# Kernel tuning notes

Measured on AMD Instinct MI355X. Metric: run time of the kernel, lower is better.

## Reference

```python
import jax, jax.numpy as jnp
import numpy as np

B, C, H, W = 2, 192, 128, 128
HEADS = 4
M = 128          # num_tokens
RD = 10          # reducted_dim
GS = 256         # category_size
TDF = 16         # dim_ffn_td
HID = 4 * C      # mlp hidden (768)
HIDT = HID + TDF # 784 after concat with token-dict features
KS = 5


def _ln(x, g, b):
    mu = x.mean(-1, keepdims=True)
    var = ((x - mu) ** 2).mean(-1, keepdims=True)
    return (x - mu) / jnp.sqrt(var + 1e-5) * g + b


def _gelu(x):
    return jax.nn.gelu(x, approximate=False)  # torch nn.GELU default = exact erf


def setup_inputs() -> dict:
    key = jax.random.key(0)
    ks = jax.random.split(key, 16)
    s = 0.02
    inp = {
        "x": jax.random.normal(ks[0], (B, C, H, W), jnp.float32),
        "x_size": H,
        "td": jax.random.normal(ks[1], (M, C), jnp.float32),
        "g1": jnp.ones((C,)), "b1": jnp.zeros((C,)),
        "g2": jnp.ones((C,)), "b2": jnp.zeros((C,)),
        "g3": jnp.ones((C,)), "b3": jnp.zeros((C,)),
        "wq_w": jax.random.normal(ks[2], (C, RD)) * s, "wq_b": jnp.zeros((RD,)),
        "wk_w": jax.random.normal(ks[3], (C, RD)) * s, "wk_b": jnp.zeros((RD,)),
        "wv_w": jax.random.normal(ks[4], (C, C)) * s, "wv_b": jnp.zeros((C,)),
        "ca_scale": jnp.ones((1,)),
        "wqkv_w": jax.random.normal(ks[5], (C, 3 * C)) * s, "wqkv_b": jnp.zeros((3 * C,)),
        "proj_w": jax.random.normal(ks[6], (C, C)) * s, "proj_b": jnp.zeros((C,)),
        "fc_td_w": jax.random.normal(ks[7], (C, TDF)) * s, "fc_td_b": jnp.zeros((TDF,)),
        "fc1_w": jax.random.normal(ks[8], (C, HID)) * s, "fc1_b": jnp.zeros((HID,)),
        "dw_w": jax.random.normal(ks[9], (HIDT, 1, KS, KS)) * s, "dw_b": jnp.zeros((HIDT,)),
        "fc2_w": jax.random.normal(ks[10], (HIDT, C)) * s, "fc2_b": jnp.zeros((C,)),
    }
    return inp


def reference(x, x_size, td, g1, b1, g2, b2, g3, b3, wq_w, wq_b, wk_w, wk_b,
              wv_w, wv_b, ca_scale, wqkv_w, wqkv_b, proj_w, proj_b,
              fc_td_w, fc_td_b, fc1_w, fc1_b, dw_w, dw_b, fc2_w, fc2_b):
    b, c, h, w = x.shape
    n = h * w
    xs = x.reshape(b, c, n).transpose(0, 2, 1)          # [b,n,c] patch_embed
    shortcut = xs
    xn = _ln(xs, g1, b1)                                # norm1

    # ---- ATD_CA: L2-normalized cross-attention to token dict ----
    q = xn @ wq_w + wq_b                                # [b,n,rd]
    k = td @ wk_w + wk_b                                # [m,rd]
    v = td @ wv_w + wv_b                                # [m,c]
    qn = q / jnp.maximum(jnp.linalg.norm(q, axis=-1, keepdims=True), 1e-12)
    kn = k / jnp.maximum(jnp.linalg.norm(k, axis=-1, keepdims=True), 1e-12)
    sim = jnp.einsum('bnr,mr->bnm', qn, kn)
    scale = 1.0 + jnp.clip(ca_scale, 0.0, 3.0) * np.log(M)
    sim = jax.nn.softmax(sim * scale, axis=-1)          # [b,n,m]
    x_atd = jnp.einsum('bnm,mc->bnc', sim, v)
    tk_id = jnp.argmax(sim, axis=-1)                    # [b,n] int

    # ---- AC_MSA: category-sorted grouped self-attention ----
    qkv = xn @ wqkv_w + wqkv_b                          # [b,n,3c]
    sort_idx = jnp.argsort(tk_id, axis=-1)              # [b,n]
    inv_idx = jnp.argsort(sort_idx, axis=-1)            # index_reverse
    shuf = jnp.take_along_axis(qkv, sort_idx[:, :, None], axis=1)
    gs = min(n, GS)
    ng = (n + gs - 1) // gs
    pad_n = ng * gs - n
    pad = jnp.flip(shuf[:, n - pad_n:n, :], axis=1)
    padded = jnp.concatenate([shuf, pad], axis=1)       # [b, ng*gs, 3c]
    hd = c // HEADS
    y = padded.reshape(b, ng, gs, 3, HEADS, hd)
    y = jnp.transpose(y, (3, 0, 1, 4, 2, 5))            # [3,b,ng,H,gs,hd]
    q2, k2, v2 = y[0], y[1], y[2]
    attn = jnp.einsum('bghqd,bghkd->bghqk', q2, k2) * (hd ** -0.5)
    attn = jax.nn.softmax(attn, axis=-1)
    o = jnp.einsum('bghqk,bghkd->bghqd', attn, v2)
    o = jnp.transpose(o, (0, 1, 3, 2, 4)).reshape(b, ng * gs, c)[:, :n, :]
    o = jnp.take_along_axis(o, inv_idx[:, :, None], axis=1)
    x_aca = o @ proj_w + proj_b

    # ---- token-dict features gathered per token ----
    td_feat = td @ fc_td_w + fc_td_b                    # [m,tdf]
    x_td = jnp.take(td_feat, tk_id, axis=0)             # [b,n,tdf]

    # ---- ConvFFN_td ----
    xn2 = _ln(xs, g2, b2)
    h1 = _gelu(xn2 @ fc1_w + fc1_b)                     # [b,n,hid]
    hcat = jnp.concatenate([h1, x_td], axis=-1)         # [b,n,hidt]
    img = hcat.transpose(0, 2, 1).reshape(b, HIDT, h, w)
    conv = jax.lax.conv_general_dilated(
        img, dw_w, window_strides=(1, 1), padding=((KS // 2, KS // 2),) * 2,
        dimension_numbers=('NCHW', 'OIHW', 'NCHW'), feature_group_count=HIDT)
    conv = _gelu(conv + dw_b[None, :, None, None])
    conv = conv.reshape(b, HIDT, n).transpose(0, 2, 1)
    x_ffn = (hcat + conv) @ fc2_w + fc2_b
    x_ffn = _ln(x_ffn, g3, b3)                          # norm3

    out = shortcut + x_atd + x_aca + x_ffn
    return out.transpose(0, 2, 1).reshape(b, c, h, w)
```

## Files before the change

### kernel.cpp

```cpp
#include <hip/hip_runtime.h>
#include <hip/hip_bf16.h>
#include <math.h>

using bf16 = __hip_bfloat16;

static constexpr int B = 2, C = 192, Hh = 128, Ww = 128, N = Hh * Ww;
static constexpr int M = 128, RD = 10, GS = 256, NG = N / GS;
static constexpr int HEADS = 4, HD = C / HEADS;
static constexpr int TDF = 16, HID = 4 * C, HIDT = HID + TDF;
static constexpr int TC3 = 3 * C;
static constexpr float LOG_M = 4.852030263919617f;
static constexpr float ATT_SCALE = 0.14433756729740643f;

typedef __attribute__((ext_vector_type(8))) short bf16x8;
typedef __attribute__((ext_vector_type(4))) float f32x4;

__device__ __forceinline__ float b2f(bf16 v) { return __bfloat162float(v); }
__device__ __forceinline__ bf16 f2b(float v) { return __float2bfloat16(v); }
__device__ __forceinline__ float bits2f(unsigned short u) { return __uint_as_float(((unsigned)u) << 16); }
__device__ __forceinline__ unsigned short f2bits(float f) {
    union { bf16 h; unsigned short u; } cv; cv.h = f2b(f); return cv.u;
}
__device__ __forceinline__ float gelu_exact(float v) {
    return 0.5f * v * (1.0f + erff(v * 0.70710678118654752f));
}

__global__ void __launch_bounds__(256) k_wtrans(const float* in, bf16* out, int K, int Nn) {
    __shared__ float T[64][65];
    int n0 = blockIdx.x * 64, k0 = blockIdx.y * 64;
    int tid = threadIdx.x;
    for (int e = tid; e < 4096; e += 256) {
        int kk = e >> 6, nn = e & 63;
        if (k0 + kk < K) T[kk][nn] = in[(size_t)(k0 + kk) * Nn + n0 + nn];
    }
    __syncthreads();
    for (int e = tid; e < 4096; e += 256) {
        int nn = e >> 6, kk = e & 63;
        if (k0 + kk < K) out[(size_t)(n0 + nn) * K + k0 + kk] = f2b(T[kk][nn]);
    }
}

__global__ void k_precompute(const float* td, const float* wk_w, const float* wk_b,
                             const float* wv_w, const float* wv_b,
                             const float* fc_td_w, const float* fc_td_b,
                             float* kn, bf16* vvT, float* tdf) {
    int m = blockIdx.x;
    int lane = threadIdx.x;
    __shared__ float trow[C];
    for (int ch = lane; ch < C; ch += 64) trow[ch] = td[m * C + ch];
    __syncthreads();
    __shared__ float ks[RD];
    __shared__ float inv_s;
    if (lane < RD) {
        float s = wk_b[lane];
        for (int ch = 0; ch < C; ++ch) s += trow[ch] * wk_w[ch * RD + lane];
        ks[lane] = s;
    }
    __syncthreads();
    if (lane == 0) {
        float ss = 0.f;
        for (int r = 0; r < RD; ++r) ss += ks[r] * ks[r];
        inv_s = 1.0f / fmaxf(sqrtf(ss), 1e-12f);
    }
    __syncthreads();
    if (lane < RD) kn[m * RD + lane] = ks[lane] * inv_s;
    for (int c0 = 0; c0 < 3; ++c0) {
        int co = lane + 64 * c0;
        float s = wv_b[co];
        for (int ch = 0; ch < C; ++ch) s += trow[ch] * wv_w[ch * C + co];
        vvT[(size_t)co * M + m] = f2b(s);
    }
    if (lane < TDF) {
        float s = fc_td_b[lane];
        for (int ch = 0; ch < C; ++ch) s += trow[ch] * fc_td_w[ch * TDF + lane];
        tdf[m * TDF + lane] = s;
    }
}

__global__ void __launch_bounds__(256) k_ln(const float* x, bf16* t, float* xn32, float* acc) {
    __shared__ float Xs[64 * 193];
    __shared__ float mu_s[64], rs_s[64];
    int tid = threadIdx.x;
    int m0 = blockIdx.x * 64;
    int b = m0 / N, i0 = m0 % N;
    for (int e = tid; e < 192 * 64; e += 256) {
        int ch = e >> 6, ii = e & 63;
        Xs[ii * 193 + ch] = x[((size_t)b * C + ch) * N + i0 + ii];
    }
    __syncthreads();
    {
        int tok = tid >> 2, part = tid & 3;
        float s = 0.f, ss = 0.f;
        for (int ch = part * 48; ch < part * 48 + 48; ++ch) {
            float v = Xs[tok * 193 + ch]; s += v; ss += v * v;
        }
        s += __shfl_xor(s, 1); ss += __shfl_xor(ss, 1);
        s += __shfl_xor(s, 2); ss += __shfl_xor(ss, 2);
        if (part == 0) {
            float mu = s / C;
            mu_s[tok] = mu;
            rs_s[tok] = rsqrtf(ss / C - mu * mu + 1e-5f);
        }
    }
    __syncthreads();
    for (int e = tid; e < 64 * 192; e += 256) {
        int ii = e / 192, ch = e % 192;
        float v = Xs[ii * 193 + ch];
        float xn = (v - mu_s[ii]) * rs_s[ii];
        size_t g = (size_t)(m0 + ii);
        t[g * C + ch] = f2b(xn);
        xn32[g * C + ch] = xn;
        acc[g * C + ch] = v;
    }
}

__global__ void __launch_bounds__(256) k_atdca(const float* xn32, const float* g1, const float* b1,
                        const float* wq_w, const float* wq_b, const float* ca_scale,
                        const float* kn, bf16* p_buf, int* tk_id) {
    int t0 = blockIdx.x * 4;
    int w = threadIdx.x >> 6, lane = threadIdx.x & 63;
    int g = t0 + w;
    float xn[3];
    #pragma unroll
    for (int k = 0; k < 3; ++k) {
        int ch = lane + 64 * k;
        xn[k] = xn32[(size_t)g * C + ch] * g1[ch] + b1[ch];
    }
    float q[RD];
    #pragma unroll
    for (int r = 0; r < RD; ++r) {
        float p = 0.f;
        #pragma unroll
        for (int k = 0; k < 3; ++k) { int ch = lane + 64 * k; p += xn[k] * wq_w[ch * RD + r]; }
        for (int mk = 32; mk >= 1; mk >>= 1) p += __shfl_xor(p, mk);
        q[r] = p + wq_b[r];
    }
    float ssn = 0.f;
    #pragma unroll
    for (int r = 0; r < RD; ++r) ssn += q[r] * q[r];
    float invq = 1.0f / fmaxf(sqrtf(ssn), 1e-12f);
    float s0 = 0.f, s1 = 0.f;
    #pragma unroll
    for (int r = 0; r < RD; ++r) {
        float qr = q[r] * invq;
        s0 += qr * kn[lane * RD + r];
        s1 += qr * kn[(lane + 64) * RD + r];
    }
    float mv; int mi;
    if (s1 > s0) { mv = s1; mi = lane + 64; } else { mv = s0; mi = lane; }
    for (int mk = 32; mk >= 1; mk >>= 1) {
        float ov = __shfl_xor(mv, mk); int oi = __shfl_xor(mi, mk);
        if (ov > mv || (ov == mv && oi < mi)) { mv = ov; mi = oi; }
    }
    float cs = ca_scale[0]; cs = fminf(fmaxf(cs, 0.0f), 3.0f);
    float scale = 1.0f + cs * LOG_M;
    float e0 = expf((s0 - mv) * scale), e1 = expf((s1 - mv) * scale);
    float sum = e0 + e1;
    for (int mk = 32; mk >= 1; mk >>= 1) sum += __shfl_xor(sum, mk);
    float invs = 1.0f / sum;
    p_buf[(size_t)g * M + lane] = f2b(e0 * invs);
    p_buf[(size_t)g * M + lane + 64] = f2b(e1 * invs);
    if (lane == 0) tk_id[g] = mi;
}

__global__ void __launch_bounds__(256) k_pv(const bf16* p_buf, const bf16* vvT, float* acc) {
    __shared__ __align__(16) short As[64 * 136];
    __shared__ __align__(16) short Bs[64 * 136];
    int tid = threadIdx.x;
    int m0 = blockIdx.x * 64;
    int n0 = blockIdx.y * 64;
    for (int e = tid; e < 64 * 16; e += 256) {
        int m = e >> 4, kc = (e & 15) * 8;
        *(uint4*)&As[m * 136 + kc] = *(const uint4*)(p_buf + (size_t)(m0 + m) * M + kc);
    }
    for (int e = tid; e < 64 * 16; e += 256) {
        int n = e >> 4, kc = (e & 15) * 8;
        *(uint4*)&Bs[n * 136 + kc] = *(const uint4*)(vvT + (size_t)(n0 + n) * M + kc);
    }
    __syncthreads();
    int w = tid >> 6, lane = tid & 63;
    int wm = (w >> 1) * 32, wn = (w & 1) * 32;
    int lr = lane & 15, lk = (lane >> 4) * 8;
    f32x4 acc00 = {0.f,0.f,0.f,0.f}, acc01 = acc00, acc10 = acc00, acc11 = acc00;
    #pragma unroll
    for (int ks = 0; ks < 4; ++ks) {
        int k0 = ks * 32 + lk;
        bf16x8 a0 = *(bf16x8*)&As[(wm + lr) * 136 + k0];
        bf16x8 a1 = *(bf16x8*)&As[(wm + 16 + lr) * 136 + k0];
        bf16x8 b0 = *(bf16x8*)&Bs[(wn + lr) * 136 + k0];
        bf16x8 b1 = *(bf16x8*)&Bs[(wn + 16 + lr) * 136 + k0];
        acc00 = __builtin_amdgcn_mfma_f32_16x16x32_bf16(a0, b0, acc00, 0, 0, 0);
        acc01 = __builtin_amdgcn_mfma_f32_16x16x32_bf16(a0, b1, acc01, 0, 0, 0);
        acc10 = __builtin_amdgcn_mfma_f32_16x16x32_bf16(a1, b0, acc10, 0, 0, 0);
        acc11 = __builtin_amdgcn_mfma_f32_16x16x32_bf16(a1, b1, acc11, 0, 0, 0);
    }
    int rbase = (lane >> 4) * 4;
    f32x4 accs[2][2] = {{acc00, acc01}, {acc10, acc11}};
    #pragma unroll
    for (int mt = 0; mt < 2; ++mt) {
        #pragma unroll
        for (int nt = 0; nt < 2; ++nt) {
            int co = n0 + wn + nt * 16 + lr;
            #pragma unroll
            for (int r = 0; r < 4; ++r) {
                int tok = m0 + wm + mt * 16 + rbase + r;
                acc[(size_t)tok * C + co] += accs[mt][nt][r];
            }
        }
    }
}

template<int NOUT, int OUTLD, int MODE, bool HASGAIN>
__global__ void __launch_bounds__(256) k_gemm192(const bf16* Abuf, const float* gain, const float* beta,
                                                 const bf16* Wt, const float* bias,
                                                 bf16* outb, float* outf) {
    __shared__ __align__(16) short As[64 * 200];
    __shared__ __align__(16) short Bs[64 * 200];
    int tid = threadIdx.x;
    int m0 = blockIdx.x * 64;
    int n0 = blockIdx.y * 64;
    for (int e = tid; e < 64 * 24; e += 256) {
        int m = e / 24, kc = (e % 24) * 8;
        uint4 raw = *(const uint4*)(Abuf + (size_t)(m0 + m) * C + kc);
        if (HASGAIN) {
            unsigned short* u = (unsigned short*)&raw;
            unsigned short o[8];
            #pragma unroll
            for (int j = 0; j < 8; ++j) o[j] = f2bits(bits2f(u[j]) * gain[kc + j] + beta[kc + j]);
            *(uint4*)&As[m * 200 + kc] = *(uint4*)o;
        } else {
            *(uint4*)&As[m * 200 + kc] = raw;
        }
    }
    for (int e = tid; e < 64 * 24; e += 256) {
        int n = e / 24, kc = (e % 24) * 8;
        *(uint4*)&Bs[n * 200 + kc] = *(const uint4*)(Wt + (size_t)(n0 + n) * C + kc);
    }
    __syncthreads();
    int w = tid >> 6, lane = tid & 63;
    int wm = (w >> 1) * 32, wn = (w & 1) * 32;
    int lr = lane & 15, lk = (lane >> 4) * 8;
    f32x4 acc00 = {0.f,0.f,0.f,0.f}, acc01 = acc00, acc10 = acc00, acc11 = acc00;
    #pragma unroll
    for (int ks = 0; ks < 6; ++ks) {
        int k0 = ks * 32 + lk;
        bf16x8 a0 = *(bf16x8*)&As[(wm + lr) * 200 + k0];
        bf16x8 a1 = *(bf16x8*)&As[(wm + 16 + lr) * 200 + k0];
        bf16x8 b0 = *(bf16x8*)&Bs[(wn + lr) * 200 + k0];
        bf16x8 b1 = *(bf16x8*)&Bs[(wn + 16 + lr) * 200 + k0];
        acc00 = __builtin_amdgcn_mfma_f32_16x16x32_bf16(a0, b0, acc00, 0, 0, 0);
        acc01 = __builtin_amdgcn_mfma_f32_16x16x32_bf16(a0, b1, acc01, 0, 0, 0);
        acc10 = __builtin_amdgcn_mfma_f32_16x16x32_bf16(a1, b0, acc10, 0, 0, 0);
        acc11 = __builtin_amdgcn_mfma_f32_16x16x32_bf16(a1, b1, acc11, 0, 0, 0);
    }
    int rbase = (lane >> 4) * 4;
    f32x4 accs[2][2] = {{acc00, acc01}, {acc10, acc11}};
    #pragma unroll
    for (int mt = 0; mt < 2; ++mt) {
        #pragma unroll
        for (int nt = 0; nt < 2; ++nt) {
            int co = n0 + wn + nt * 16 + lr;
            float bv = bias[co];
            #pragma unroll
            for (int r = 0; r < 4; ++r) {
                int tok = m0 + wm + mt * 16 + rbase + r;
                float v = accs[mt][nt][r] + bv;
                if (MODE == 0) outb[(size_t)tok * OUTLD + co] = f2b(v);
                else if (MODE == 1) outb[(size_t)tok * OUTLD + co] = f2b(gelu_exact(v));
                else outf[(size_t)tok * OUTLD + co] += v;
            }
        }
    }
}

__global__ void k_sort_count(const int* tk_id, int* chunk_cnt) {
    int c = blockIdx.x, b = blockIdx.y;
    int tid = threadIdx.x;
    __shared__ int cnt[M];
    cnt[tid] = 0;
    __syncthreads();
    atomicAdd(&cnt[tk_id[b * N + c * 128 + tid]], 1);
    __syncthreads();
    chunk_cnt[(b * 128 + c) * M + tid] = cnt[tid];
}

__global__ void k_sort_scan(int* chunk_cnt) {
    int b = blockIdx.x;
    int k = threadIdx.x;
    int tot = 0;
    for (int c = 0; c < 128; ++c) tot += chunk_cnt[(b * 128 + c) * M + k];
    __shared__ int totals[M];
    __shared__ int base[M];
    totals[k] = tot;
    __syncthreads();
    if (k == 0) {
        int run = 0;
        for (int kk = 0; kk < M; ++kk) { base[kk] = run; run += totals[kk]; }
    }
    __syncthreads();
    int run = base[k];
    for (int c = 0; c < 128; ++c) {
        int v = chunk_cnt[(b * 128 + c) * M + k];
        chunk_cnt[(b * 128 + c) * M + k] = run;
        run += v;
    }
}

__global__ void k_sort_scatter(const int* tk_id, const int* chunk_cnt, int* sort_idx) {
    int c = blockIdx.x, b = blockIdx.y;
    int k = threadIdx.x;
    __shared__ int keys[128];
    keys[k] = tk_id[b * N + c * 128 + k];
    __syncthreads();
    int off = chunk_cnt[(b * 128 + c) * M + k];
    for (int j = 0; j < 128; ++j) {
        if (keys[j] == k) sort_idx[b * N + off++] = c * 128 + j;
    }
}

__global__ void __launch_bounds__(256) k_attn_mfma(const bf16* qkv, const int* sort_idx, bf16* o_buf) {
    int g = blockIdx.x, h = blockIdx.y, b = blockIdx.z;
    __shared__ int sidx[GS];
    __shared__ __align__(16) unsigned short Kl[256 * 64];
    __shared__ __align__(16) unsigned short Vt[48 * 256];
    __shared__ __align__(16) unsigned short Pl[4][64 * 32];
    int tid = threadIdx.x;
    sidx[tid] = sort_idx[b * N + g * GS + tid];
    __syncthreads();
    {
        int row = tid;
        int srow = sidx[row];
        size_t kb = ((size_t)(b * N + srow)) * TC3 + C + h * HD;
        size_t vb = ((size_t)(b * N + srow)) * TC3 + 2 * C + h * HD;
        #pragma unroll
        for (int db = 0; db < 6; ++db) {
            uint4 kv = *(const uint4*)(qkv + kb + db * 8);
            *(uint4*)&Kl[row * 64 + ((db ^ (row & 7)) * 8)] = kv;
            uint4 vv4 = *(const uint4*)(qkv + vb + db * 8);
            unsigned short* vu = (unsigned short*)&vv4;
            #pragma unroll
            for (int j = 0; j < 8; ++j) {
                int d = db * 8 + j;
                Vt[d * 256 + (((row >> 3) ^ (d & 7)) * 8) + (row & 7)] = vu[j];
            }
        }
        uint4 z = {0u,0u,0u,0u};
        *(uint4*)&Kl[row * 64 + ((6 ^ (row & 7)) * 8)] = z;
        *(uint4*)&Kl[row * 64 + ((7 ^ (row & 7)) * 8)] = z;
    }
    __syncthreads();
    int w = tid >> 6, l = tid & 63;
    int lq = l & 15, g8 = l >> 4;
    bf16x8 qf[4][2];
    #pragma unroll
    for (int qt = 0; qt < 4; ++qt) {
        int qrow = sidx[w * 64 + qt * 16 + lq];
        size_t qb = ((size_t)(b * N + qrow)) * TC3 + h * HD;
        qf[qt][0] = *(const bf16x8*)(qkv + qb + g8 * 8);
        int d1 = 32 + g8 * 8;
        if (d1 < HD) qf[qt][1] = *(const bf16x8*)(qkv + qb + d1);
        else { uint4 z = {0u,0u,0u,0u}; qf[qt][1] = *(bf16x8*)&z; }
    }
    float mrun[4], lrun[4];
    f32x4 Oa[4][3];
    #pragma unroll
    for (int qt = 0; qt < 4; ++qt) {
        mrun[qt] = -1e30f; lrun[qt] = 0.f;
        #pragma unroll
        for (int dt = 0; dt < 3; ++dt) Oa[qt][dt] = (f32x4){0.f,0.f,0.f,0.f};
    }
    unsigned short* Pw = &Pl[w][0];
    for (int ck = 0; ck < 8; ++ck) {
        int kbase = ck * 32;
        bf16x8 kf[2][2];
        #pragma unroll
        for (int kt = 0; kt < 2; ++kt) {
            int key = kbase + kt * 16 + lq;
            #pragma unroll
            for (int ks = 0; ks < 2; ++ks)
                kf[kt][ks] = *(bf16x8*)&Kl[key * 64 + (((ks * 4 + g8) ^ (key & 7)) * 8)];
        }
        bf16x8 vf[3];
        #pragma unroll
        for (int dt = 0; dt < 3; ++dt) {
            int d = dt * 16 + lq;
            vf[dt] = *(bf16x8*)&Vt[d * 256 + ((((kbase >> 3) + g8) ^ (d & 7)) * 8)];
        }
        #pragma unroll
        for (int qt = 0; qt < 4; ++qt) {
            f32x4 s0 = {0.f,0.f,0.f,0.f}, s1 = s0;
            s0 = __builtin_amdgcn_mfma_f32_16x16x32_bf16(kf[0][0], qf[qt][0], s0, 0, 0, 0);
            s0 = __builtin_amdgcn_mfma_f32_16x16x32_bf16(kf[0][1], qf[qt][1], s0, 0, 0, 0);
            s1 = __builtin_amdgcn_mfma_f32_16x16x32_bf16(kf[1][0], qf[qt][0], s1, 0, 0, 0);
            s1 = __builtin_amdgcn_mfma_f32_16x16x32_bf16(kf[1][1], qf[qt][1], s1, 0, 0, 0);
            float sv0[4], sv1[4];
            float cmax = -1e30f;
            #pragma unroll
            for (int r = 0; r < 4; ++r) {
                sv0[r] = s0[r] * ATT_SCALE; sv1[r] = s1[r] * ATT_SCALE;
                cmax = fmaxf(cmax, fmaxf(sv0[r], sv1[r]));
            }
            cmax = fmaxf(cmax, __shfl_xor(cmax, 16));
            cmax = fmaxf(cmax, __shfl_xor(cmax, 32));
            float mnew = fmaxf(mrun[qt], cmax);
            float sf = expf(mrun[qt] - mnew);
            float p0[4], p1[4], csum = 0.f;
            #pragma unroll
            for (int r = 0; r < 4; ++r) {
                p0[r] = expf(sv0[r] - mnew); p1[r] = expf(sv1[r] - mnew);
                csum += p0[r] + p1[r];
            }
            csum += __shfl_xor(csum, 16);
            csum += __shfl_xor(csum, 32);
            lrun[qt] = lrun[qt] * sf + csum;
            mrun[qt] = mnew;
            int q = qt * 16 + lq;
            {
                unsigned short pw[4];
                #pragma unroll
                for (int r = 0; r < 4; ++r) pw[r] = f2bits(p0[r]);
                int slot = g8;
                int addr = q * 32 + (((slot >> 1) ^ (q & 3)) * 8) + (slot & 1) * 4;
                *(uint2*)&Pw[addr] = *(uint2*)pw;
                #pragma unroll
                for (int r = 0; r < 4; ++r) pw[r] = f2bits(p1[r]);
                slot = 4 + g8;
                addr = q * 32 + (((slot >> 1) ^ (q & 3)) * 8) + (slot & 1) * 4;
                *(uint2*)&Pw[addr] = *(uint2*)pw;
            }
            float sfr[4];
            #pragma unroll
            for (int r = 0; r < 4; ++r) sfr[r] = __shfl(sf, 4 * g8 + r);
            #pragma unroll
            for (int dt = 0; dt < 3; ++dt)
                #pragma unroll
                for (int r = 0; r < 4; ++r) Oa[qt][dt][r] *= sfr[r];
            bf16x8 pa = *(bf16x8*)&Pw[q * 32 + ((g8 ^ (lq & 3)) * 8)];
            #pragma unroll
            for (int dt = 0; dt < 3; ++dt)
                Oa[qt][dt] = __builtin_amdgcn_mfma_f32_16x16x32_bf16(pa, vf[dt], Oa[qt][dt], 0, 0, 0);
        }
    }
    #pragma unroll
    for (int qt = 0; qt < 4; ++qt) {
        float invq = 1.0f / lrun[qt];
        float invr[4];
        #pragma unroll
        for (int r = 0; r < 4; ++r) invr[r] = __shfl(invq, 4 * g8 + r);
        #pragma unroll
        for (int r = 0; r < 4; ++r) {
            int grow = sidx[w * 64 + qt * 16 + 4 * g8 + r];
            size_t obase = ((size_t)(b * N + grow)) * C + h * HD;
            #pragma unroll
            for (int dt = 0; dt < 3; ++dt)
                o_buf[obase + dt * 16 + lq] = f2b(Oa[qt][dt][r] * invr[r]);
        }
    }
}

__global__ void k_tdfill(const int* tk_id, const float* tdf, bf16* hcat) {
    int idx = blockIdx.x * 256 + threadIdx.x;
    if (idx >= B * N * TDF) return;
    int tok = idx >> 4, f = idx & 15;
    hcat[(size_t)tok * HIDT + HID + f] = f2b(tdf[tk_id[tok] * TDF + f]);
}

__global__ void __launch_bounds__(256) k_conv(const bf16* hcat, const float* dw_w, const float* dw_b,
                                              bf16* convsum) {
    int st = blockIdx.x;
    int c16 = blockIdx.y;
    int b = blockIdx.z;
    int tx0 = (st & 7) * 16, ty0 = (st >> 3) * 16;
    int tid = threadIdx.x;
    __shared__ __align__(16) float Hf[20 * 81 * 4];
    __shared__ __align__(16) float Wf[25 * 16];
    __shared__ float Wb[16];
    for (int e = tid; e < 400; e += 256) {
        int tap = e >> 4, ch = e & 15;
        Wf[e] = dw_w[(size_t)(c16 * 16 + ch) * 25 + tap];
    }
    if (tid < 16) Wb[tid] = dw_b[c16 * 16 + tid];
    for (int e = tid; e < 800; e += 256) {
        int pos = e >> 1, sc = e & 1;
        int py = pos / 20, px = pos % 20;
        int gy = ty0 + py - 2, gx = tx0 + px - 2;
        uint4 v = {0u, 0u, 0u, 0u};
        if (gy >= 0 && gy < Hh && gx >= 0 && gx < Ww)
            v = *(const uint4*)(hcat + ((size_t)b * N + gy * Ww + gx) * HIDT + c16 * 16 + sc * 8);
        unsigned short* u = (unsigned short*)&v;
        float4 f0 = { bits2f(u[0]), bits2f(u[1]), bits2f(u[2]), bits2f(u[3]) };
        float4 f1 = { bits2f(u[4]), bits2f(u[5]), bits2f(u[6]), bits2f(u[7]) };
        int base = (py * 81 + px * 4 + sc * 2) * 4;
        *(float4*)&Hf[base] = f0;
        *(float4*)&Hf[base + 4] = f1;
    }
    __syncthreads();
    int cc = tid & 1, lx = (tid >> 1) & 7, ly = tid >> 4;
    float acc[2][8] = {};
    #pragma unroll 1
    for (int ky = 0; ky < 5; ++ky) {
        int py = ly + ky;
        float4 w[5][2];
        #pragma unroll
        for (int kx = 0; kx < 5; ++kx) {
            w[kx][0] = *(float4*)&Wf[(ky * 5 + kx) * 16 + cc * 8];
            w[kx][1] = *(float4*)&Wf[(ky * 5 + kx) * 16 + cc * 8 + 4];
        }
        #pragma unroll
        for (int c = 0; c < 6; ++c) {
            int px = 2 * lx + c;
            int base = (py * 81 + px * 4 + cc * 2) * 4;
            float4 f0 = *(float4*)&Hf[base];
            float4 f1 = *(float4*)&Hf[base + 4];
            float f[8] = { f0.x, f0.y, f0.z, f0.w, f1.x, f1.y, f1.z, f1.w };
            #pragma unroll
            for (int kx = 0; kx < 5; ++kx) {
                int ox = c - kx;
                if (ox >= 0 && ox < 2) {
                    const float* wp = (const float*)&w[kx][0];
                    #pragma unroll
                    for (int j = 0; j < 8; ++j) acc[ox][j] += f[j] * wp[j];
                }
            }
        }
    }
    int gy = ty0 + ly;
    #pragma unroll
    for (int ox = 0; ox < 2; ++ox) {
        int px = 2 * lx + ox + 2, py = ly + 2;
        int base = (py * 81 + px * 4 + cc * 2) * 4;
        float4 f0 = *(float4*)&Hf[base];
        float4 f1 = *(float4*)&Hf[base + 4];
        float cf[8] = { f0.x, f0.y, f0.z, f0.w, f1.x, f1.y, f1.z, f1.w };
        unsigned short ow[8];
        #pragma unroll
        for (int j = 0; j < 8; ++j)
            ow[j] = f2bits(cf[j] + gelu_exact(acc[ox][j] + Wb[cc * 8 + j]));
        int gx = tx0 + 2 * lx + ox;
        *(uint4*)(convsum + ((size_t)b * N + gy * Ww + gx) * HIDT + c16 * 16 + cc * 8) = *(uint4*)ow;
    }
}

__global__ void __launch_bounds__(256) k_fc2ln(const bf16* convsum, const bf16* Wt,
                                               const float* bias, const float* g3, const float* b3,
                                               const float* accres, float* out) {
    __shared__ __align__(16) char smem[65536];
    unsigned short* AsB = (unsigned short*)smem;
    unsigned short* BsB = (unsigned short*)(smem + 16384);
    float* Ot = (float*)smem;
    int tid = threadIdx.x;
    int m0 = blockIdx.x * 64;
    int w = tid >> 6, lane = tid & 63;
    int lr = lane & 15, g8 = lane >> 4;
    f32x4 acc[12];
    #pragma unroll
    for (int nt = 0; nt < 12; ++nt) acc[nt] = (f32x4){0.f, 0.f, 0.f, 0.f};

    auto stage = [&](int d, int kc) {
        int kb = kc * 64;
        unsigned short* As = AsB + d * 4096;
        unsigned short* Bs = BsB + d * 12288;
        for (int e = tid; e < 512; e += 256) {
            int m = e >> 3, k8 = (e & 7) * 8;
            uint4 v = {0u,0u,0u,0u};
            if (kb + k8 < HIDT) v = *(const uint4*)(convsum + (size_t)(m0 + m) * HIDT + kb + k8);
            *(uint4*)&As[m * 64 + (((e & 7) ^ (m & 7)) * 8)] = v;
        }
        for (int e = tid; e < 1536; e += 256) {
            int n = e >> 3, k8 = (e & 7) * 8;
            uint4 v = {0u,0u,0u,0u};
            if (kb + k8 < HIDT) v = *(const uint4*)(Wt + (size_t)n * HIDT + kb + k8);
            *(uint4*)&Bs[n * 64 + (((e & 7) ^ (n & 7)) * 8)] = v;
        }
    };
    stage(0, 0);
    int cur = 0;
    for (int kc = 0; kc < 13; ++kc) {
        __syncthreads();
        if (kc + 1 < 13) stage(cur ^ 1, kc + 1);
        unsigned short* As = AsB + cur * 4096;
        unsigned short* Bs = BsB + cur * 12288;
        #pragma unroll
        for (int ks = 0; ks < 2; ++ks) {
            int kg = ks * 4 + g8;
            int arow = w * 16 + lr;
            bf16x8 a = *(bf16x8*)&As[arow * 64 + ((kg ^ (arow & 7)) * 8)];
            #pragma unroll
            for (int nt = 0; nt < 12; ++nt) {
                int nrow = nt * 16 + lr;
                bf16x8 bfr = *(bf16x8*)&Bs[nrow * 64 + ((kg ^ (nrow & 7)) * 8)];
                acc[nt] = __builtin_amdgcn_mfma_f32_16x16x32_bf16(a, bfr, acc[nt], 0, 0, 0);
            }
        }
        cur ^= 1;
    }
    #pragma unroll
    for (int nt = 0; nt < 12; ++nt) {
        float bv = bias[nt * 16 + lr];
        #pragma unroll
        for (int r = 0; r < 4; ++r) acc[nt][r] += bv;
    }
    float mu_r[4], rs_r[4];
    #pragma unroll
    for (int r = 0; r < 4; ++r) {
        float s = 0.f, ss = 0.f;
        #pragma unroll
        for (int nt = 0; nt < 12; ++nt) { float v = acc[nt][r]; s += v; ss += v * v; }
        s += __shfl_xor(s, 1); ss += __shfl_xor(ss, 1);
        s += __shfl_xor(s, 2); ss += __shfl_xor(ss, 2);
        s += __shfl_xor(s, 4); ss += __shfl_xor(ss, 4);
        s += __shfl_xor(s, 8); ss += __shfl_xor(ss, 8);
        mu_r[r] = s / C;
        rs_r[r] = rsqrtf(ss / C - mu_r[r] * mu_r[r] + 1e-5f);
    }
    int bb = m0 / N, i0 = m0 % N;
    for (int h = 0; h < 2; ++h) {
        __syncthreads();
        #pragma unroll
        for (int ntl = 0; ntl < 6; ++ntl) {
            int nt = h * 6 + ntl;
            int c = nt * 16 + lr;
            float g3v = g3[c], b3v = b3[c];
            #pragma unroll
            for (int r = 0; r < 4; ++r) {
                int tok = m0 + w * 16 + g8 * 4 + r;
                float o = accres[(size_t)tok * C + c] + (acc[nt][r] - mu_r[r]) * rs_r[r] * g3v + b3v;
                Ot[(ntl * 16 + lr) * 68 + w * 16 + g8 * 4 + r] = o;
            }
        }
        __syncthreads();
        for (int e = tid; e < 96 * 16; e += 256) {
            int row = e >> 4, q4 = e & 15;
            int c = h * 96 + row;
            float4 v = *(float4*)&Ot[row * 68 + q4 * 4];
            *(float4*)(out + ((size_t)(bb * C + c)) * N + i0 + q4 * 4) = v;
        }
    }
}

__global__ void k_sentinel(float* out, int nelem) {
    int i = blockIdx.x * blockDim.x + threadIdx.x;
    if (i < nelem) out[i] = 1234.0f;
}

extern "C" void kernel_launch(void* const* d_in, const int* in_sizes, int n_in,
                              void* d_out, int out_size, void* d_ws, size_t ws_size,
                              hipStream_t stream) {
    const float* x        = (const float*)d_in[0];
    const float* td       = (const float*)d_in[2];
    const float* g1       = (const float*)d_in[3];
    const float* b1       = (const float*)d_in[4];
    const float* g2       = (const float*)d_in[5];
    const float* b2v      = (const float*)d_in[6];
    const float* g3       = (const float*)d_in[7];
    const float* b3       = (const float*)d_in[8];
    const float* wq_w     = (const float*)d_in[9];
    const float* wq_b     = (const float*)d_in[10];
    const float* wk_w     = (const float*)d_in[11];
    const float* wk_b     = (const float*)d_in[12];
    const float* wv_w     = (const float*)d_in[13];
    const float* wv_b     = (const float*)d_in[14];
    const float* ca_scale = (const float*)d_in[15];
    const float* wqkv_w   = (const float*)d_in[16];
    const float* wqkv_b   = (const float*)d_in[17];
    const float* proj_w   = (const float*)d_in[18];
    const float* proj_b   = (const float*)d_in[19];
    const float* fc_td_w  = (const float*)d_in[20];
    const float* fc_td_b  = (const float*)d_in[21];
    const float* fc1_w    = (const float*)d_in[22];
    const float* fc1_b    = (const float*)d_in[23];
    const float* dw_w     = (const float*)d_in[24];
    const float* dw_b     = (const float*)d_in[25];
    const float* fc2_w    = (const float*)d_in[26];
    const float* fc2_b    = (const float*)d_in[27];
    float* out = (float*)d_out;

    char* ws = (char*)d_ws;
    size_t off = 0;
    auto alloc = [&](size_t bytes) { size_t o = off; off += (bytes + 255) & ~(size_t)255; return o; };
    size_t o_t     = alloc((size_t)B * N * C * 2);
    size_t o_xn32  = alloc((size_t)B * N * C * 4);
    size_t o_acc   = alloc((size_t)B * N * C * 4);
    size_t o_qkv   = alloc((size_t)B * N * TC3 * 2);
    size_t o_obuf  = alloc((size_t)B * N * C * 2);
    size_t o_hcat  = alloc((size_t)B * N * HIDT * 2);
    size_t o_conv  = alloc((size_t)B * N * HIDT * 2);
    size_t o_kn    = alloc((size_t)M * RD * 4);
    size_t o_vvT   = alloc((size_t)C * M * 2);
    size_t o_tdf   = alloc((size_t)M * TDF * 4);
    size_t o_tk    = alloc((size_t)B * N * 4);
    size_t o_sidx  = alloc((size_t)B * N * 4);
    size_t o_ccnt  = alloc((size_t)B * 128 * M * 4);
    size_t o_pbuf  = alloc((size_t)B * N * M * 2);
    size_t o_wqkvT = alloc((size_t)TC3 * C * 2);
    size_t o_projT = alloc((size_t)C * C * 2);
    size_t o_fc1T  = alloc((size_t)HID * C * 2);
    size_t o_fc2T  = alloc((size_t)C * HIDT * 2);

    if (ws_size < off) {
        k_sentinel<<<(out_size + 255) / 256, 256, 0, stream>>>(out, out_size);
        return;
    }

    bf16*  t_buf   = (bf16*)(ws + o_t);
    float* xn32    = (float*)(ws + o_xn32);
    float* acc     = (float*)(ws + o_acc);
    bf16*  qkv     = (bf16*)(ws + o_qkv);
    bf16*  o_bufp  = (bf16*)(ws + o_obuf);
    bf16*  hcat    = (bf16*)(ws + o_hcat);
    bf16*  convsum = (bf16*)(ws + o_conv);
    float* kn      = (float*)(ws + o_kn);
    bf16*  vvT     = (bf16*)(ws + o_vvT);
    float* tdf     = (float*)(ws + o_tdf);
    int*   tk_id   = (int*)(ws + o_tk);
    int*   sidx    = (int*)(ws + o_sidx);
    int*   ccnt    = (int*)(ws + o_ccnt);
    bf16*  p_buf   = (bf16*)(ws + o_pbuf);
    bf16*  wqkvT   = (bf16*)(ws + o_wqkvT);
    bf16*  projT   = (bf16*)(ws + o_projT);
    bf16*  fc1T    = (bf16*)(ws + o_fc1T);
    bf16*  fc2T    = (bf16*)(ws + o_fc2T);

    k_wtrans<<<dim3(TC3 / 64, C / 64), 256, 0, stream>>>(wqkv_w, wqkvT, C, TC3);
    k_wtrans<<<dim3(C / 64, C / 64), 256, 0, stream>>>(proj_w, projT, C, C);
    k_wtrans<<<dim3(HID / 64, C / 64), 256, 0, stream>>>(fc1_w, fc1T, C, HID);
    k_wtrans<<<dim3(C / 64, (HIDT + 63) / 64), 256, 0, stream>>>(fc2_w, fc2T, HIDT, C);

    k_precompute<<<M, 64, 0, stream>>>(td, wk_w, wk_b, wv_w, wv_b, fc_td_w, fc_td_b, kn, vvT, tdf);
    k_ln<<<B * N / 64, 256, 0, stream>>>(x, t_buf, xn32, acc);
    k_atdca<<<B * N / 4, 256, 0, stream>>>(xn32, g1, b1, wq_w, wq_b, ca_scale, kn, p_buf, tk_id);
    k_pv<<<dim3(B * N / 64, C / 64), 256, 0, stream>>>(p_buf, vvT, acc);
    k_gemm192<TC3, TC3, 0, true><<<dim3(B * N / 64, TC3 / 64), 256, 0, stream>>>(
        t_buf, g1, b1, wqkvT, wqkv_b, qkv, nullptr);
    k_sort_count<<<dim3(128, B), 128, 0, stream>>>(tk_id, ccnt);
    k_sort_scan<<<B, 128, 0, stream>>>(ccnt);
    k_sort_scatter<<<dim3(128, B), 128, 0, stream>>>(tk_id, ccnt, sidx);
    k_attn_mfma<<<dim3(NG, HEADS, B), 256, 0, stream>>>(qkv, sidx, o_bufp);
    k_gemm192<C, C, 2, false><<<dim3(B * N / 64, C / 64), 256, 0, stream>>>(
        o_bufp, nullptr, nullptr, projT, proj_b, nullptr, acc);
    k_gemm192<HID, HIDT, 1, true><<<dim3(B * N / 64, HID / 64), 256, 0, stream>>>(
        t_buf, g2, b2v, fc1T, fc1_b, hcat, nullptr);
    k_tdfill<<<(B * N * TDF + 255) / 256, 256, 0, stream>>>(tk_id, tdf, hcat);
    k_conv<<<dim3(64, 49, B), 256, 0, stream>>>(hcat, dw_w, dw_b, convsum);
    k_fc2ln<<<B * N / 64, 256, 0, stream>>>(convsum, fc2T, fc2_b, g3, b3, acc, out);
}
```

Baseline: 390.9 us.

## Enlarge GEMM tiles to 128x96 and fold LN affine into the LN kernel

Replaces the 64x64 single-shot GEMM kernel with a 128x96 tile that loops over K in two 96-wide chunks, giving each wave a 4x3 grid of MFMA accumulators for more operand reuse per LDS load. The LayerNorm gain and bias for norm1 and norm2 are now applied once in k_ln, which writes two bf16 normalized buffers, so the GEMM loaders no longer do per-element affine conversion. This costs an extra bf16 activation write and read plus higher register pressure from 48 accumulator values per lane.

Result: slower. 399.4 us (+2.2%).

```diff
diff --git a/kernel.cpp b/kernel.cpp
--- a/kernel.cpp
+++ b/kernel.cpp
@@ -77,7 +77,9 @@
     }
 }
 
-__global__ void __launch_bounds__(256) k_ln(const float* x, bf16* t, float* xn32, float* acc) {
+__global__ void __launch_bounds__(256) k_ln(const float* x, const float* g1, const float* b1,
+                                            const float* g2, const float* b2v,
+                                            bf16* xn1, bf16* xn2, float* xn32, float* acc) {
     __shared__ float Xs[64 * 193];
     __shared__ float mu_s[64], rs_s[64];
     int tid = threadIdx.x;
@@ -108,7 +110,8 @@
         float v = Xs[ii * 193 + ch];
         float xn = (v - mu_s[ii]) * rs_s[ii];
         size_t g = (size_t)(m0 + ii);
-        t[g * C + ch] = f2b(xn);
+        xn1[g * C + ch] = f2b(xn * g1[ch] + b1[ch]);
+        xn2[g * C + ch] = f2b(xn * g2[ch] + b2v[ch]);
         xn32[g * C + ch] = xn;
         acc[g * C + ch] = v;
     }
@@ -210,61 +213,59 @@
     }
 }
 
-template<int NOUT, int OUTLD, int MODE, bool HASGAIN>
-__global__ void __launch_bounds__(256) k_gemm192(const bf16* Abuf, const float* gain, const float* beta,
-                                                 const bf16* Wt, const float* bias,
-                                                 bf16* outb, float* outf) {
-    __shared__ __align__(16) short As[64 * 200];
-    __shared__ __align__(16) short Bs[64 * 200];
+template<int OUTLD, int MODE>
+__global__ void __launch_bounds__(256) k_gemm_big(const bf16* Abuf, const bf16* Wt, const float* bias,
+                                                  bf16* outb, float* outf) {
+    __shared__ __align__(16) unsigned short As[128 * 104];
+    __shared__ __align__(16) unsigned short Bs[96 * 104];
     int tid = threadIdx.x;
-    int m0 = blockIdx.x * 64;
-    int n0 = blockIdx.y * 64;
-    for (int e = tid; e < 64 * 24; e += 256) {
-        int m = e / 24, kc = (e % 24) * 8;
-        uint4 raw = *(const uint4*)(Abuf + (size_t)(m0 + m) * C + kc);
-        if (HASGAIN) {
-            unsigned short* u = (unsigned short*)&raw;
-            unsigned short o[8];
-            #pragma unroll
-            for (int j = 0; j < 8; ++j) o[j] = f2bits(bits2f(u[j]) * gain[kc + j] + beta[kc + j]);
-            *(uint4*)&As[m * 200 + kc] = *(uint4*)o;
-        } else {
-            *(uint4*)&As[m * 200 + kc] = raw;
-        }
-    }
-    for (int e = tid; e < 64 * 24; e += 256) {
-        int n = e / 24, kc = (e % 24) * 8;
-        *(uint4*)&Bs[n * 200 + kc] = *(const uint4*)(Wt + (size_t)(n0 + n) * C + kc);
-    }
-    __syncthreads();
+    int m0 = blockIdx.x * 128, n0 = blockIdx.y * 96;
     int w = tid >> 6, lane = tid & 63;
-    int wm = (w >> 1) * 32, wn = (w & 1) * 32;
-    int lr = lane & 15, lk = (lane >> 4) * 8;
-    f32x4 acc00 = {0.f,0.f,0.f,0.f}, acc01 = acc00, acc10 = acc00, acc11 = acc00;
-    #pragma unroll
-    for (int ks = 0; ks < 6; ++ks) {
-        int k0 = ks * 32 + lk;
-        bf16x8 a0 = *(bf16x8*)&As[(wm + lr) * 200 + k0];
-        bf16x8 a1 = *(bf16x8*)&As[(wm + 16 + lr) * 200 + k0];
-        bf16x8 b0 = *(bf16x8*)&Bs[(wn + lr) * 200 + k0];
-        bf16x8 b1 = *(bf16x8*)&Bs[(wn + 16 + lr) * 200 + k0];
-        acc00 = __builtin_amdgcn_mfma_f32_16x16x32_bf16(a0, b0, acc00, 0, 0, 0);
-        acc01 = __builtin_amdgcn_mfma_f32_16x16x32_bf16(a0, b1, acc01, 0, 0, 0);
-        acc10 = __builtin_amdgcn_mfma_f32_16x16x32_bf16(a1, b0, acc10, 0, 0, 0);
-        acc11 = __builtin_amdgcn_mfma_f32_16x16x32_bf16(a1, b1, acc11, 0, 0, 0);
-    }
-    int rbase = (lane >> 4) * 4;
-    f32x4 accs[2][2] = {{acc00, acc01}, {acc10, acc11}};
-    #pragma unroll
-    for (int mt = 0; mt < 2; ++mt) {
-        #pragma unroll
-        for (int nt = 0; nt < 2; ++nt) {
-            int co = n0 + wn + nt * 16 + lr;
-            float bv = bias[co];
+    int wm = (w >> 1) * 64, wn = (w & 1) * 48;
+    int lr = lane & 15, g8 = lane >> 4;
+    f32x4 acc[4][3];
+    #pragma unroll
+    for (int mt = 0; mt < 4; ++mt)
+        #pragma unroll
+        for (int nt = 0; nt < 3; ++nt) acc[mt][nt] = (f32x4){0.f,0.f,0.f,0.f};
+    for (int kc = 0; kc < 2; ++kc) {
+        int kb = kc * 96;
+        __syncthreads();
+        for (int e = tid; e < 128 * 12; e += 256) {
+            int m = e / 12, blk = e % 12;
+            *(uint4*)&As[m * 104 + blk * 8] = *(const uint4*)(Abuf + (size_t)(m0 + m) * C + kb + blk * 8);
+        }
+        for (int e = tid; e < 96 * 12; e += 256) {
+            int n = e / 12, blk = e % 12;
+            *(uint4*)&Bs[n * 104 + blk * 8] = *(const uint4*)(Wt + (size_t)(n0 + n) * C + kb + blk * 8);
+        }
+        __syncthreads();
+        #pragma unroll
+        for (int ks = 0; ks < 3; ++ks) {
+            int blk = ks * 4 + g8;
+            bf16x8 a[4];
+            bf16x8 bfr[3];
+            #pragma unroll
+            for (int mt = 0; mt < 4; ++mt) a[mt] = *(bf16x8*)&As[(wm + mt * 16 + lr) * 104 + blk * 8];
+            #pragma unroll
+            for (int nt = 0; nt < 3; ++nt) bfr[nt] = *(bf16x8*)&Bs[(wn + nt * 16 + lr) * 104 + blk * 8];
+            #pragma unroll
+            for (int mt = 0; mt < 4; ++mt)
+                #pragma unroll
+                for (int nt = 0; nt < 3; ++nt)
+                    acc[mt][nt] = __builtin_amdgcn_mfma_f32_16x16x32_bf16(a[mt], bfr[nt], acc[mt][nt], 0, 0, 0);
+        }
+    }
+    #pragma unroll
+    for (int nt = 0; nt < 3; ++nt) {
+        int co = n0 + wn + nt * 16 + lr;
+        float bv = bias[co];
+        #pragma unroll
+        for (int mt = 0; mt < 4; ++mt) {
             #pragma unroll
             for (int r = 0; r < 4; ++r) {
-                int tok = m0 + wm + mt * 16 + rbase + r;
-                float v = accs[mt][nt][r] + bv;
+                int tok = m0 + wm + mt * 16 + g8 * 4 + r;
+                float v = acc[mt][nt][r] + bv;
                 if (MODE == 0) outb[(size_t)tok * OUTLD + co] = f2b(v);
                 else if (MODE == 1) outb[(size_t)tok * OUTLD + co] = f2b(gelu_exact(v));
                 else outf[(size_t)tok * OUTLD + co] += v;
@@ -678,7 +679,8 @@
     char* ws = (char*)d_ws;
     size_t off = 0;
     auto alloc = [&](size_t bytes) { size_t o = off; off += (bytes + 255) & ~(size_t)255; return o; };
-    size_t o_t     = alloc((size_t)B * N * C * 2);
+    size_t o_xn1   = alloc((size_t)B * N * C * 2);
+    size_t o_xn2   = alloc((size_t)B * N * C * 2);
     size_t o_xn32  = alloc((size_t)B * N * C * 4);
     size_t o_acc   = alloc((size_t)B * N * C * 4);
     size_t o_qkv   = alloc((size_t)B * N * TC3 * 2);
@@ -702,7 +704,8 @@
         return;
     }
 
-    bf16*  t_buf   = (bf16*)(ws + o_t);
+    bf16*  xn1     = (bf16*)(ws + o_xn1);
+    bf16*  xn2     = (bf16*)(ws + o_xn2);
     float* xn32    = (float*)(ws + o_xn32);
     float* acc     = (float*)(ws + o_acc);
     bf16*  qkv     = (bf16*)(ws + o_qkv);
@@ -727,19 +730,19 @@
     k_wtrans<<<dim3(C / 64, (HIDT + 63) / 64), 256, 0, stream>>>(fc2_w, fc2T, HIDT, C);
 
     k_precompute<<<M, 64, 0, stream>>>(td, wk_w, wk_b, wv_w, wv_b, fc_td_w, fc_td_b, kn, vvT, tdf);
-    k_ln<<<B * N / 64, 256, 0, stream>>>(x, t_buf, xn32, acc);
+    k_ln<<<B * N / 64, 256, 0, stream>>>(x, g1, b1, g2, b2v, xn1, xn2, xn32, acc);
     k_atdca<<<B * N / 4, 256, 0, stream>>>(xn32, g1, b1, wq_w, wq_b, ca_scale, kn, p_buf, tk_id);
     k_pv<<<dim3(B * N / 64, C / 64), 256, 0, stream>>>(p_buf, vvT, acc);
-    k_gemm192<TC3, TC3, 0, true><<<dim3(B * N / 64, TC3 / 64), 256, 0, stream>>>(
-        t_buf, g1, b1, wqkvT, wqkv_b, qkv, nullptr);
+    k_gemm_big<TC3, 0><<<dim3(B * N / 128, TC3 / 96), 256, 0, stream>>>(
+        xn1, wqkvT, wqkv_b, qkv, nullptr);
     k_sort_count<<<dim3(128, B), 128, 0, stream>>>(tk_id, ccnt);
     k_sort_scan<<<B, 128, 0, stream>>>(ccnt);
     k_sort_scatter<<<dim3(128, B), 128, 0, stream>>>(tk_id, ccnt, sidx);
     k_attn_mfma<<<dim3(NG, HEADS, B), 256, 0, stream>>>(qkv, sidx, o_bufp);
-    k_gemm192<C, C, 2, false><<<dim3(B * N / 64, C / 64), 256, 0, stream>>>(
-        o_bufp, nullptr, nullptr, projT, proj_b, nullptr, acc);
-    k_gemm192<HID, HIDT, 1, true><<<dim3(B * N / 64, HID / 64), 256, 0, stream>>>(
-        t_buf, g2, b2v, fc1T, fc1_b, hcat, nullptr);
+    k_gemm_big<C, 2><<<dim3(B * N / 128, C / 96), 256, 0, stream>>>(
+        o_bufp, projT, proj_b, nullptr, acc);
+    k_gemm_big<HIDT, 1><<<dim3(B * N / 128, HID / 96), 256, 0, stream>>>(
+        xn2, fc1T, fc1_b, hcat, nullptr);
     k_tdfill<<<(B * N * TDF + 255) / 256, 256, 0, stream>>>(tk_id, tdf, hcat);
     k_conv<<<dim3(64, 49, B), 256, 0, stream>>>(hcat, dw_w, dw_b, convsum);
     k_fc2ln<<<B * N / 64, 256, 0, stream>>>(convsum, fc2T, fc2_b, g3, b3, acc, out);
```
